# Optimization experiments

Hardware: AMD Instinct MI355X
Metric: run time of the kernel (lower is better)

The kernel has to match this reference:

```python
import jax, jax.numpy as jnp
import numpy as np

N_NODES = 50000
N_EDGES_UND = 400000
N_GRAPHS = 128
LATENT = 64
OUT_DIM = 64
NODE_F = 64
EDGE_F = 32
MAX_LV = 3


def setup_inputs() -> dict:
    key = jax.random.key(0)
    ks = jax.random.split(key, 12)
    rng = np.random.default_rng(0)
    # Build consistent directed edge list: each undirected pair (u,v) yields
    # directed edges e (u->v) and e+E_und (v->u); rev maps each to its twin.
    u = rng.integers(0, N_NODES, size=N_EDGES_UND)
    v = rng.integers(0, N_NODES, size=N_EDGES_UND)
    src = jnp.asarray(np.concatenate([u, v]), dtype=jnp.int32)
    dst = jnp.asarray(np.concatenate([v, u]), dtype=jnp.int32)
    e = np.arange(N_EDGES_UND)
    rev = jnp.asarray(np.concatenate([e + N_EDGES_UND, e]), dtype=jnp.int32)
    graph_ids = jnp.sort(jax.random.randint(ks[0], (N_NODES,), 0, N_GRAPHS)).astype(jnp.int32)
    s = 0.05
    return {
        'node_feat': jax.random.normal(ks[1], (N_NODES, NODE_F), jnp.float32),
        'edge_feat': jax.random.normal(ks[2], (2 * N_EDGES_UND, EDGE_F), jnp.float32),
        'src': src, 'dst': dst, 'rev': rev,
        'graph_ids': graph_ids, 'n_graphs': N_GRAPHS,
        'Wn': jax.random.normal(ks[3], (NODE_F, LATENT), jnp.float32) * s,
        'bn': jnp.zeros((LATENT,), jnp.float32),
        'We': jax.random.normal(ks[4], (EDGE_F, LATENT), jnp.float32) * s,
        'be': jnp.zeros((LATENT,), jnp.float32),
        'Wc': jax.random.normal(ks[5], (LATENT, LATENT), jnp.float32) * s,
        'bc': jnp.zeros((LATENT,), jnp.float32),
        'Wo': jax.random.normal(ks[6], (LATENT, OUT_DIM), jnp.float32) * s,
        'bo': jnp.zeros((OUT_DIM,), jnp.float32),
    }


def reference(node_feat, edge_feat, src, dst, rev, graph_ids, n_graphs,
              Wn, bn, We, be, Wc, bc, Wo, bo):
    n_nodes = node_feat.shape[0]
    # w_n2l / w_e2l
    input_node_linear = node_feat @ Wn + bn                  # [N, D]
    input_edge_linear = edge_feat @ We + be                  # [E, D]
    # n2e spmm: each directed edge gathers its source node's row
    input_message = input_edge_linear + input_node_linear[src]  # [E, D]
    cur = jax.nn.relu(input_message)
    # loopy BP: e2e spmm = (sum of messages into src node) - reverse-edge message
    for _ in range(MAX_LV):
        node_agg = jax.ops.segment_sum(cur, dst, num_segments=n_nodes)  # [N, D]
        e2epool = node_agg[src] - cur[rev]                              # [E, D]
        cur = jax.nn.relu(e2epool @ Wc + bc + input_message)
    # e2n spmm: sum incoming edge messages per node
    e2npool = jax.ops.segment_sum(cur, dst, num_segments=n_nodes)       # [N, D]
    hidden_msg = jax.nn.relu(e2npool)
    reluact = jax.nn.relu(hidden_msg @ Wo + bo)                         # [N, out]
    # subg spmm: sum node outputs per graph
    y = jax.ops.segment_sum(reluact, graph_ids, num_segments=n_graphs)  # [G, out]
    return jax.nn.relu(y)
```

## Files before the change

### kernel.cpp

```cpp
#include <hip/hip_runtime.h>


#define NN 50000
#define NE 800000
#define NG 128
#define D 64
#define LDE 36
#define LDW 66
#define LDO 72

typedef unsigned short u16;
typedef unsigned int u32;
typedef __bf16 bf16x8 __attribute__((ext_vector_type(8)));
typedef float f32x4 __attribute__((ext_vector_type(4)));

__device__ __forceinline__ float b2f(u16 u){ u32 x=((u32)u)<<16; float f; __builtin_memcpy(&f,&x,4); return f; }
__device__ __forceinline__ u16 f2b(float f){ u32 x; __builtin_memcpy(&x,&f,4); x += 0x7fffu + ((x>>16)&1u); return (u16)(x>>16); }
__device__ __forceinline__ u32 pack2(float a, float b){ return (u32)f2b(a) | ((u32)f2b(b)<<16); }
__device__ __forceinline__ void unpack8(uint4 v, float* o){
  o[0]=b2f((u16)(v.x&0xffffu)); o[1]=b2f((u16)(v.x>>16));
  o[2]=b2f((u16)(v.y&0xffffu)); o[3]=b2f((u16)(v.y>>16));
  o[4]=b2f((u16)(v.z&0xffffu)); o[5]=b2f((u16)(v.z>>16));
  o[6]=b2f((u16)(v.w&0xffffu)); o[7]=b2f((u16)(v.w>>16));
}

__global__ __launch_bounds__(256) void k_prep(const float* __restrict__ Wc, const float* __restrict__ We,
                                              u16* __restrict__ wcT, u16* __restrict__ weT){
  int i = blockIdx.x*256 + threadIdx.x;
  if (i < 4096){ int n=i>>6, k=i&63; wcT[i] = f2b(Wc[k*D+n]); }
  int j = i - 4096;
  if (j >= 0 && j < 2048){ int n=j>>5, k=j&31; weT[j] = f2b(We[k*D+n]); }
}

template<int ZERO>
__global__ __launch_bounds__(256) void k_cvt(const float* __restrict__ srcv, u16* __restrict__ dstb,
                                             float* __restrict__ zbuf){
  size_t i = (size_t)(blockIdx.x*256 + threadIdx.x)*4;
  float4 v = *(const float4*)(srcv + i);
  *(uint2*)(dstb + i) = make_uint2(pack2(v.x,v.y), pack2(v.z,v.w));
  if (ZERO) *(float4*)(zbuf + i) = make_float4(0.f,0.f,0.f,0.f);
}

__global__ __launch_bounds__(256) void k_inl(const float* __restrict__ nf, const float* __restrict__ Wn,
                                             const float* __restrict__ bn, u16* __restrict__ inlb){
  __shared__ float w[D*D];
  for (int i=threadIdx.x;i<D*D;i+=256) w[i]=Wn[i];
  __syncthreads();
  const int d = threadIdx.x&63;
  const int n = blockIdx.x*4 + (threadIdx.x>>6);
  if (n>=NN) return;
  float v = bn[d];
  const float* row = nf + (size_t)n*D;
  #pragma unroll 8
  for (int k=0;k<D;k++) v += row[k]*w[k*D+d];
  inlb[(size_t)n*D+d] = f2b(v);
}

__global__ __launch_bounds__(256) void k_im(const float* __restrict__ ef, const u16* __restrict__ weT,
                                            const float* __restrict__ be, const u16* __restrict__ inlb,
                                            const int* __restrict__ src, const int* __restrict__ perm,
                                            u16* __restrict__ imP){
  __shared__ __align__(16) u16 efs[64*LDE];
  __shared__ __align__(16) u16 wts[64*LDE];
  __shared__ float os[64*68];
  const int t = threadIdx.x;
  const int ebase = blockIdx.x*64;
  {
    int n=t&63, k0=(t>>6)*8;
    *(uint4*)&wts[n*LDE + k0] = *(const uint4*)(weT + n*32 + k0);
  }
  {
    int e=t>>2, k0=(t&3)*8;
    const float* p = ef + (size_t)(ebase+e)*32 + k0;
    float4 v0=*(const float4*)p, v1=*(const float4*)(p+4);
    uint4 pk = make_uint4(pack2(v0.x,v0.y),pack2(v0.z,v0.w),pack2(v1.x,v1.y),pack2(v1.z,v1.w));
    *(uint4*)&efs[e*LDE + k0] = pk;
  }
  __syncthreads();
  {
    int w=t>>6, lane=t&63, q=lane>>4, mr=lane&15;
    int rowb=w*16;
    bf16x8 A = *(const bf16x8*)&efs[(rowb+mr)*LDE + q*8];
    #pragma unroll
    for (int nt=0;nt<4;nt++){
      bf16x8 B = *(const bf16x8*)&wts[(nt*16+mr)*LDE + q*8];
      f32x4 acc = {0.f,0.f,0.f,0.f};
      acc = __builtin_amdgcn_mfma_f32_16x16x32_bf16(A,B,acc,0,0,0);
      #pragma unroll
      for (int r=0;r<4;r++) os[(rowb+q*4+r)*68 + nt*16+mr] = acc[r];
    }
  }
  {
    int e=t>>2, d0=(t&3)*16;
    const size_t eg = (size_t)(ebase+e);
    const int s = src[eg], ps = perm[eg];
    const u16* ip = inlb + (size_t)s*D + d0;
    uint4 iv0 = *(const uint4*)ip, iv1 = *(const uint4*)(ip+8);
    float il[16]; unpack8(iv0,il); unpack8(iv1,il+8);
    float x[16];
    #pragma unroll
    for (int j=0;j<16;j++) x[j] = os[e*68 + d0 + j] + be[d0+j] + il[j];
    uint4 p0 = make_uint4(pack2(x[0],x[1]),pack2(x[2],x[3]),pack2(x[4],x[5]),pack2(x[6],x[7]));
    uint4 p1 = make_uint4(pack2(x[8],x[9]),pack2(x[10],x[11]),pack2(x[12],x[13]),pack2(x[14],x[15]));
    u16* op = imP + (size_t)ps*D + d0;
    *(uint4*)op = p0; *(uint4*)(op+8) = p1;
  }
}

template<int MODE>
__global__ __launch_bounds__(256) void k_iter(const u16* __restrict__ imP, const u16* __restrict__ revIn,
      const u16* __restrict__ naWb, const u16* __restrict__ wcT, const float* __restrict__ bc,
      const int* __restrict__ srcP, const int* __restrict__ prevP, const int* __restrict__ nodeP,
      u16* __restrict__ revOut, float* __restrict__ naW_out){
  __shared__ __align__(16) u16 xs[64*LDW];
  __shared__ __align__(16) u16 wts[64*LDW];
  __shared__ __align__(16) u16 os[64*LDO];
  __shared__ int nid[64];
  const int t = threadIdx.x;
  const int lane = t&63, w = t>>6;
  const size_t sbase = (size_t)blockIdx.x*64;
  {
    const int k0 = w*16;
    *(uint4*)&wts[lane*LDW + k0]     = *(const uint4*)(wcT + lane*64 + k0);
    *(uint4*)&wts[lane*LDW + k0 + 8] = *(const uint4*)(wcT + lane*64 + k0 + 8);
  }
  if (lane < 16) nid[w*16 + lane] = nodeP[sbase + w*16 + lane];
  __syncthreads();
  {
    const int e = t>>2, d0 = (t&3)*16;
    const size_t slot = sbase + e;
    const u16* ip = imP + slot*D + d0;
    uint4 r0 = *(const uint4*)ip, r1 = *(const uint4*)(ip+8);
    float x[16]; unpack8(r0,x); unpack8(r1,x+8);
    if (MODE == 1){
      const int sp = srcP[slot];
      const u16* cp = revIn + slot*D + d0;
      uint4 c0=*(const uint4*)cp, c1=*(const uint4*)(cp+8);
      const u16* np_ = naWb + (size_t)sp*D + d0;
      uint4 n0=*(const uint4*)np_, n1=*(const uint4*)(np_+8);
      float cv[16], nv[16];
      unpack8(c0,cv); unpack8(c1,cv+8);
      unpack8(n0,nv); unpack8(n1,nv+8);
      #pragma unroll
      for (int j=0;j<16;j++) x[j] += nv[j] - cv[j] + bc[d0+j];
    }
    #pragma unroll
    for (int j=0;j<16;j++) x[j] = x[j]>0.f ? x[j] : 0.f;
    uint4 p0 = make_uint4(pack2(x[0],x[1]),pack2(x[2],x[3]),pack2(x[4],x[5]),pack2(x[6],x[7]));
    uint4 p1 = make_uint4(pack2(x[8],x[9]),pack2(x[10],x[11]),pack2(x[12],x[13]),pack2(x[14],x[15]));
    u16* qd = &xs[e*LDW + d0];
    *(uint4*)qd = p0; *(uint4*)(qd+8) = p1;
  }
  {
    const int q = lane>>4, mr = lane&15;
    const int rowb = w*16;
    bf16x8 A0 = *(const bf16x8*)&xs[(rowb+mr)*LDW + q*8];
    bf16x8 A1 = *(const bf16x8*)&xs[(rowb+mr)*LDW + 32 + q*8];
    #pragma unroll
    for (int nt=0;nt<4;nt++){
      bf16x8 B0 = *(const bf16x8*)&wts[(nt*16+mr)*LDW + q*8];
      bf16x8 B1 = *(const bf16x8*)&wts[(nt*16+mr)*LDW + 32 + q*8];
      f32x4 acc = {0.f,0.f,0.f,0.f};
      acc = __builtin_amdgcn_mfma_f32_16x16x32_bf16(A0,B0,acc,0,0,0);
      acc = __builtin_amdgcn_mfma_f32_16x16x32_bf16(A1,B1,acc,0,0,0);
      #pragma unroll
      for (int r=0;r<4;r++) os[(rowb+q*4+r)*LDO + nt*16 + mr] = f2b(acc[r]);
    }
    const int lr = lane>>2, cc = lane&3;
    const int tgt = prevP[sbase + rowb + lr];
    u16* gp = revOut + (size_t)tgt*D + cc*16;
    *(uint4*)gp     = *(const uint4*)&os[(rowb+lr)*LDO + cc*16];
    *(uint4*)(gp+8) = *(const uint4*)&os[(rowb+lr)*LDO + cc*16 + 8];
    float acc = 0.f;
    int curn = nid[rowb];
    #pragma unroll 4
    for (int i=0;i<16;++i){
      int n = nid[rowb+i];
      if (n != curn){
        atomicAdd(&naW_out[(size_t)curn*D + lane], acc);
        curn = n; acc = 0.f;
      }
      acc += b2f(os[(rowb+i)*LDO + lane]);
    }
    atomicAdd(&naW_out[(size_t)curn*D + lane], acc);
  }
}

__global__ __launch_bounds__(256) void k_last(const u16* __restrict__ imP, const u16* __restrict__ revIn,
      const u16* __restrict__ naWb, const float* __restrict__ bc,
      const int* __restrict__ srcP, const int* __restrict__ nodeP,
      float* __restrict__ e2n){
  __shared__ __align__(16) u16 xs[64*LDW];
  __shared__ int nid[64];
  const int t = threadIdx.x;
  const int lane = t&63, w = t>>6;
  const size_t sbase = (size_t)blockIdx.x*64;
  if (lane < 16) nid[w*16+lane] = nodeP[sbase + w*16 + lane];
  {
    const int e = t>>2, d0 = (t&3)*16;
    const size_t slot = sbase + e;
    const u16* ip = imP + slot*D + d0;
    uint4 r0 = *(const uint4*)ip, r1 = *(const uint4*)(ip+8);
    float x[16]; unpack8(r0,x); unpack8(r1,x+8);
    const int sp = srcP[slot];
    const u16* cp = revIn + slot*D + d0;
    uint4 c0 = *(const uint4*)cp, c1 = *(const uint4*)(cp+8);
    const u16* np_ = naWb + (size_t)sp*D + d0;
    uint4 n0 = *(const uint4*)np_, n1 = *(const uint4*)(np_+8);
    float cv[16], nv[16];
    unpack8(c0,cv); unpack8(c1,cv+8);
    unpack8(n0,nv); unpack8(n1,nv+8);
    #pragma unroll
    for (int j=0;j<16;j++){ x[j] += nv[j] - cv[j] + bc[d0+j]; x[j] = x[j]>0.f ? x[j] : 0.f; }
    uint4 p0 = make_uint4(pack2(x[0],x[1]),pack2(x[2],x[3]),pack2(x[4],x[5]),pack2(x[6],x[7]));
    uint4 p1 = make_uint4(pack2(x[8],x[9]),pack2(x[10],x[11]),pack2(x[12],x[13]),pack2(x[14],x[15]));
    u16* qd = &xs[e*LDW + d0];
    *(uint4*)qd = p0; *(uint4*)(qd+8) = p1;
  }
  {
    float acc = 0.f;
    int curn = nid[w*16];
    #pragma unroll 4
    for (int i=0;i<16;++i){
      int n = nid[w*16+i];
      if (n != curn){
        atomicAdd(&e2n[(size_t)curn*D + lane], acc);
        curn = n; acc = 0.f;
      }
      acc += b2f(xs[(w*16+i)*LDW + lane]);
    }
    atomicAdd(&e2n[(size_t)curn*D + lane], acc);
  }
}

__global__ void k_hist(const int* __restrict__ dst, int* __restrict__ cnt){
  int e = blockIdx.x*256 + threadIdx.x;
  atomicAdd(&cnt[dst[e]], 1);
}
__global__ __launch_bounds__(1024) void k_scan1(const int* __restrict__ cnt, int* __restrict__ outv,
                                                int* __restrict__ bsums, int n){
  __shared__ int sh[1024];
  int i = blockIdx.x*1024 + threadIdx.x;
  int v = (i<n)? cnt[i] : 0;
  sh[threadIdx.x]=v;
  __syncthreads();
  for (int off=1; off<1024; off<<=1){
    int tv = (threadIdx.x>=(unsigned)off)? sh[threadIdx.x-off] : 0;
    __syncthreads();
    sh[threadIdx.x] += tv;
    __syncthreads();
  }
  if (i<n) outv[i] = sh[threadIdx.x] - v;
  if (threadIdx.x==1023) bsums[blockIdx.x] = sh[1023];
}
__global__ __launch_bounds__(1024) void k_scan3(int* __restrict__ off, int* __restrict__ cur,
                                                const int* __restrict__ bsums, int n){
  __shared__ int spref;
  if (threadIdx.x < 64){
    int v = ((int)threadIdx.x < (int)blockIdx.x) ? bsums[threadIdx.x] : 0;
    #pragma unroll
    for (int o=1;o<64;o<<=1) v += __shfl_xor(v, o, 64);
    if (threadIdx.x==0) spref = v;
  }
  __syncthreads();
  int i = blockIdx.x*1024 + threadIdx.x;
  if (i<n){ int v = off[i] + spref; off[i]=v; cur[i]=v; }
}
__global__ void k_fill(const int* __restrict__ dst, const int* __restrict__ src,
                       int* __restrict__ cur, int* __restrict__ perm,
                       int* __restrict__ srcP, int* __restrict__ nodeP){
  int e = blockIdx.x*256 + threadIdx.x;
  int d = dst[e];
  int pos = atomicAdd(&cur[d], 1);
  perm[e] = pos;
  srcP[pos] = src[e];
  nodeP[pos] = d;
}
__global__ void k_prev(const int* __restrict__ rev, const int* __restrict__ perm, int* __restrict__ prevP){
  int e = blockIdx.x*256 + threadIdx.x;
  prevP[perm[e]] = perm[rev[e]];
}

__global__ __launch_bounds__(256) void k_final(const float* __restrict__ e2n, const float* __restrict__ Wo,
                                               const float* __restrict__ bo, const int* __restrict__ gid,
                                               float* __restrict__ yacc){
  __shared__ float w[D*D];
  for (int i=threadIdx.x;i<D*D;i+=256) w[i]=Wo[i];
  __syncthreads();
  const int d = threadIdx.x&63, sub = threadIdx.x>>6;
  const int n0 = blockIdx.x*32 + sub*8;
  const float bod = bo[d];
  float acc=0.f; int curg=-1;
  for (int i=0;i<8;i++){
    int n=n0+i;
    if (n>=NN) break;
    int g = gid[n];
    if (g!=curg){ if (curg>=0) atomicAdd(&yacc[curg*D+d], acc); curg=g; acc=0.f; }
    float v=bod;
    const float* er = e2n + (size_t)n*D;
    #pragma unroll 8
    for (int k=0;k<D;k++){ float h=er[k]; h = h>0.f?h:0.f; v += h*w[k*D+d]; }
    acc += (v>0.f ? v : 0.f);
  }
  if (curg>=0) atomicAdd(&yacc[curg*D+d], acc);
}
__global__ void k_out(const float* __restrict__ yacc, float* __restrict__ outp){
  int i = blockIdx.x*256 + threadIdx.x;
  if (i<NG*D){ float v=yacc[i]; outp[i]= v>0.f?v:0.f; }
}

static constexpr size_t SZ_E   = (size_t)NE*D*2;
static constexpr size_t SZ_NF4 = (size_t)NN*D*4;
static constexpr size_t SZ_NB  = (size_t)NN*D*2;
static constexpr size_t OFF_IMP  = 0;
static constexpr size_t OFF_RVA  = SZ_E;
static constexpr size_t OFF_RVB  = 2*SZ_E;
static constexpr size_t OFF_CCUR = 3*SZ_E;
static constexpr size_t OFF_NA0  = OFF_CCUR + 200064;
static constexpr size_t OFF_NA1  = OFF_NA0 + SZ_NF4;
static constexpr size_t OFF_E2N  = OFF_NA1 + SZ_NF4;
static constexpr size_t OFF_YACC = OFF_E2N + SZ_NF4;
static constexpr size_t ZERO_SZ  = 200064 + 3*SZ_NF4 + (size_t)NG*D*4;
static constexpr size_t OFF_NAB  = OFF_YACC + (size_t)NG*D*4;
static constexpr size_t OFF_INL  = OFF_NAB + SZ_NB;
static constexpr size_t OFF_COFF = OFF_INL + SZ_NB;
static constexpr size_t OFF_PERM = OFF_COFF + 200064;
static constexpr size_t OFF_SRCP = OFF_PERM + (size_t)NE*4;
static constexpr size_t OFF_PRVP = OFF_SRCP + (size_t)NE*4;
static constexpr size_t OFF_NODP = OFF_PRVP + (size_t)NE*4;
static constexpr size_t OFF_BS   = OFF_NODP + (size_t)NE*4;
static constexpr size_t OFF_WCT  = OFF_BS + 256;
static constexpr size_t OFF_WET  = OFF_WCT + 8192;

extern "C" void kernel_launch(void* const* d_in, const int* in_sizes, int n_in,
                              void* d_out, int out_size, void* d_ws, size_t ws_size,
                              hipStream_t stream) {
  const float* node_feat = (const float*)d_in[0];
  const float* edge_feat = (const float*)d_in[1];
  const int*   src       = (const int*)d_in[2];
  const int*   dst       = (const int*)d_in[3];
  const int*   rev       = (const int*)d_in[4];
  const int*   gid       = (const int*)d_in[5];
  const float* Wn = (const float*)d_in[7];
  const float* bn = (const float*)d_in[8];
  const float* We = (const float*)d_in[9];
  const float* be = (const float*)d_in[10];
  const float* Wc = (const float*)d_in[11];
  const float* bc = (const float*)d_in[12];
  const float* Wo = (const float*)d_in[13];
  const float* bo = (const float*)d_in[14];

  char* ws = (char*)d_ws;
  u16*   imP     = (u16*)(ws + OFF_IMP);
  u16*   revA    = (u16*)(ws + OFF_RVA);
  u16*   revB    = (u16*)(ws + OFF_RVB);
  float* naW0    = (float*)(ws + OFF_NA0);
  float* naW1    = (float*)(ws + OFF_NA1);
  float* e2n     = (float*)(ws + OFF_E2N);
  float* yacc    = (float*)(ws + OFF_YACC);
  u16*   naWb    = (u16*)(ws + OFF_NAB);
  u16*   inlb    = (u16*)(ws + OFF_INL);
  int*   csr_off = (int*)(ws + OFF_COFF);
  int*   csr_cur = (int*)(ws + OFF_CCUR);
  int*   perm    = (int*)(ws + OFF_PERM);
  int*   srcP    = (int*)(ws + OFF_SRCP);
  int*   prevP   = (int*)(ws + OFF_PRVP);
  int*   nodeP   = (int*)(ws + OFF_NODP);
  int*   bsums   = (int*)(ws + OFF_BS);
  u16*   wcT     = (u16*)(ws + OFF_WCT);
  u16*   weT     = (u16*)(ws + OFF_WET);

  hipMemsetAsync(ws + OFF_CCUR, 0, ZERO_SZ, stream);

  k_hist <<<NE/256, 256, 0, stream>>>(dst, csr_cur);
  k_scan1<<<49, 1024, 0, stream>>>(csr_cur, csr_off, bsums, NN);
  k_scan3<<<49, 1024, 0, stream>>>(csr_off, csr_cur, bsums, NN);
  k_fill <<<NE/256, 256, 0, stream>>>(dst, src, csr_cur, perm, srcP, nodeP);
  k_prev <<<NE/256, 256, 0, stream>>>(rev, perm, prevP);

  k_prep<<<24, 256, 0, stream>>>(Wc, We, wcT, weT);
  k_inl <<<NN/4, 256, 0, stream>>>(node_feat, Wn, bn, inlb);
  k_im  <<<NE/64, 256, 0, stream>>>(edge_feat, weT, be, inlb, src, perm, imP);

  k_iter<0><<<NE/64, 256, 0, stream>>>(imP, revA, naWb, wcT, bc, srcP, prevP, nodeP, revA, naW0);
  k_cvt<0><<<3125, 256, 0, stream>>>(naW0, naWb, (float*)nullptr);
  k_iter<1><<<NE/64, 256, 0, stream>>>(imP, revA, naWb, wcT, bc, srcP, prevP, nodeP, revB, naW1);
  k_cvt<1><<<3125, 256, 0, stream>>>(naW1, naWb, naW0);
  k_iter<1><<<NE/64, 256, 0, stream>>>(imP, revB, naWb, wcT, bc, srcP, prevP, nodeP, revA, naW0);
  k_cvt<0><<<3125, 256, 0, stream>>>(naW0, naWb, (float*)nullptr);
  k_last<<<NE/64, 256, 0, stream>>>(imP, revA, naWb, bc, srcP, nodeP, e2n);

  k_final<<<(NN+31)/32, 256, 0, stream>>>(e2n, Wo, bo, gid, yacc);
  k_out<<<(NG*D)/256, 256, 0, stream>>>(yacc, (float*)d_out);
}
```

Baseline: 681.2 us.

## Drop bf16 node-aggregate conversion kernels and read MFMA weight fragments from global

Removes the three k_cvt passes that turned the fp32 node aggregates into bf16. The iteration kernels now gather the fp32 aggregate rows directly, and a memset zeroes the reused buffer instead. The weight matrices are prepacked in MFMA fragment order so each lane loads its B operand straight from global/L2, which drops the per-block shared-memory staging and a __syncthreads. The trade is twice the bytes per random node gather (fp32 instead of bf16) in exchange for fewer launches and full passes over the aggregate buffer.

Result: slower. 706.0 us (+3.6%).

```diff
diff --git a/kernel.cpp b/kernel.cpp
--- a/kernel.cpp
+++ b/kernel.cpp
@@ -25,20 +25,24 @@
 }
 
 __global__ __launch_bounds__(256) void k_prep(const float* __restrict__ Wc, const float* __restrict__ We,
-                                              u16* __restrict__ wcT, u16* __restrict__ weT){
+                                              u16* __restrict__ wcB, u16* __restrict__ weB){
   int i = blockIdx.x*256 + threadIdx.x;
-  if (i < 4096){ int n=i>>6, k=i&63; wcT[i] = f2b(Wc[k*D+n]); }
-  int j = i - 4096;
-  if (j >= 0 && j < 2048){ int n=j>>5, k=j&31; weT[j] = f2b(We[k*D+n]); }
-}
-
-template<int ZERO>
-__global__ __launch_bounds__(256) void k_cvt(const float* __restrict__ srcv, u16* __restrict__ dstb,
-                                             float* __restrict__ zbuf){
-  size_t i = (size_t)(blockIdx.x*256 + threadIdx.x)*4;
-  float4 v = *(const float4*)(srcv + i);
-  *(uint2*)(dstb + i) = make_uint2(pack2(v.x,v.y), pack2(v.z,v.w));
-  if (ZERO) *(float4*)(zbuf + i) = make_float4(0.f,0.f,0.f,0.f);
+  if (i < 4096){
+    int nt = i>>10, r = i&1023;
+    int h = r>>9, r2 = r&511;
+    int j = r2>>3, kk = r2&7;
+    int row = nt*16 + (j&15);
+    int k = h*32 + (j>>4)*8 + kk;
+    wcB[i] = f2b(Wc[k*D + row]);
+  }
+  int t = i - 4096;
+  if (t >= 0 && t < 2048){
+    int nt = t>>9, r = t&511;
+    int j = r>>3, kk = r&7;
+    int row = nt*16 + (j&15);
+    int k = (j>>4)*8 + kk;
+    weB[t] = f2b(We[k*D + row]);
+  }
 }
 
 __global__ __launch_bounds__(256) void k_inl(const float* __restrict__ nf, const float* __restrict__ Wn,
@@ -56,19 +60,14 @@
   inlb[(size_t)n*D+d] = f2b(v);
 }
 
-__global__ __launch_bounds__(256) void k_im(const float* __restrict__ ef, const u16* __restrict__ weT,
+__global__ __launch_bounds__(256) void k_im(const float* __restrict__ ef, const u16* __restrict__ weB,
                                             const float* __restrict__ be, const u16* __restrict__ inlb,
                                             const int* __restrict__ src, const int* __restrict__ perm,
                                             u16* __restrict__ imP){
   __shared__ __align__(16) u16 efs[64*LDE];
-  __shared__ __align__(16) u16 wts[64*LDE];
   __shared__ float os[64*68];
   const int t = threadIdx.x;
   const int ebase = blockIdx.x*64;
-  {
-    int n=t&63, k0=(t>>6)*8;
-    *(uint4*)&wts[n*LDE + k0] = *(const uint4*)(weT + n*32 + k0);
-  }
   {
     int e=t>>2, k0=(t&3)*8;
     const float* p = ef + (size_t)(ebase+e)*32 + k0;
@@ -76,14 +75,13 @@
     uint4 pk = make_uint4(pack2(v0.x,v0.y),pack2(v0.z,v0.w),pack2(v1.x,v1.y),pack2(v1.z,v1.w));
     *(uint4*)&efs[e*LDE + k0] = pk;
   }
-  __syncthreads();
   {
     int w=t>>6, lane=t&63, q=lane>>4, mr=lane&15;
     int rowb=w*16;
     bf16x8 A = *(const bf16x8*)&efs[(rowb+mr)*LDE + q*8];
     #pragma unroll
     for (int nt=0;nt<4;nt++){
-      bf16x8 B = *(const bf16x8*)&wts[(nt*16+mr)*LDE + q*8];
+      bf16x8 B = *(const bf16x8*)(weB + nt*512 + lane*8);
       f32x4 acc = {0.f,0.f,0.f,0.f};
       acc = __builtin_amdgcn_mfma_f32_16x16x32_bf16(A,B,acc,0,0,0);
       #pragma unroll
@@ -109,23 +107,16 @@
 
 template<int MODE>
 __global__ __launch_bounds__(256) void k_iter(const u16* __restrict__ imP, const u16* __restrict__ revIn,
-      const u16* __restrict__ naWb, const u16* __restrict__ wcT, const float* __restrict__ bc,
+      const float* __restrict__ naW, const u16* __restrict__ wcB, const float* __restrict__ bc,
       const int* __restrict__ srcP, const int* __restrict__ prevP, const int* __restrict__ nodeP,
       u16* __restrict__ revOut, float* __restrict__ naW_out){
   __shared__ __align__(16) u16 xs[64*LDW];
-  __shared__ __align__(16) u16 wts[64*LDW];
   __shared__ __align__(16) u16 os[64*LDO];
   __shared__ int nid[64];
   const int t = threadIdx.x;
   const int lane = t&63, w = t>>6;
   const size_t sbase = (size_t)blockIdx.x*64;
-  {
-    const int k0 = w*16;
-    *(uint4*)&wts[lane*LDW + k0]     = *(const uint4*)(wcT + lane*64 + k0);
-    *(uint4*)&wts[lane*LDW + k0 + 8] = *(const uint4*)(wcT + lane*64 + k0 + 8);
-  }
   if (lane < 16) nid[w*16 + lane] = nodeP[sbase + w*16 + lane];
-  __syncthreads();
   {
     const int e = t>>2, d0 = (t&3)*16;
     const size_t slot = sbase + e;
@@ -136,11 +127,15 @@
       const int sp = srcP[slot];
       const u16* cp = revIn + slot*D + d0;
       uint4 c0=*(const uint4*)cp, c1=*(const uint4*)(cp+8);
-      const u16* np_ = naWb + (size_t)sp*D + d0;
-      uint4 n0=*(const uint4*)np_, n1=*(const uint4*)(np_+8);
-      float cv[16], nv[16];
+      float nv[16];
+      { const float* np_ = naW + (size_t)sp*D + d0;
+        *(float4*)&nv[0]  = *(const float4*)np_;
+        *(float4*)&nv[4]  = *(const float4*)(np_+4);
+        *(float4*)&nv[8]  = *(const float4*)(np_+8);
+        *(float4*)&nv[12] = *(const float4*)(np_+12);
+      }
+      float cv[16];
       unpack8(c0,cv); unpack8(c1,cv+8);
-      unpack8(n0,nv); unpack8(n1,nv+8);
       #pragma unroll
       for (int j=0;j<16;j++) x[j] += nv[j] - cv[j] + bc[d0+j];
     }
@@ -158,8 +153,8 @@
     bf16x8 A1 = *(const bf16x8*)&xs[(rowb+mr)*LDW + 32 + q*8];
     #pragma unroll
     for (int nt=0;nt<4;nt++){
-      bf16x8 B0 = *(const bf16x8*)&wts[(nt*16+mr)*LDW + q*8];
-      bf16x8 B1 = *(const bf16x8*)&wts[(nt*16+mr)*LDW + 32 + q*8];
+      bf16x8 B0 = *(const bf16x8*)(wcB + nt*1024 + lane*8);
+      bf16x8 B1 = *(const bf16x8*)(wcB + nt*1024 + 512 + lane*8);
       f32x4 acc = {0.f,0.f,0.f,0.f};
       acc = __builtin_amdgcn_mfma_f32_16x16x32_bf16(A0,B0,acc,0,0,0);
       acc = __builtin_amdgcn_mfma_f32_16x16x32_bf16(A1,B1,acc,0,0,0);
@@ -187,7 +182,7 @@
 }
 
 __global__ __launch_bounds__(256) void k_last(const u16* __restrict__ imP, const u16* __restrict__ revIn,
-      const u16* __restrict__ naWb, const float* __restrict__ bc,
+      const float* __restrict__ naW, const float* __restrict__ bc,
       const int* __restrict__ srcP, const int* __restrict__ nodeP,
       float* __restrict__ e2n){
   __shared__ __align__(16) u16 xs[64*LDW];
@@ -205,11 +200,15 @@
     const int sp = srcP[slot];
     const u16* cp = revIn + slot*D + d0;
     uint4 c0 = *(const uint4*)cp, c1 = *(const uint4*)(cp+8);
-    const u16* np_ = naWb + (size_t)sp*D + d0;
-    uint4 n0 = *(const uint4*)np_, n1 = *(const uint4*)(np_+8);
-    float cv[16], nv[16];
+    float nv[16];
+    { const float* np_ = naW + (size_t)sp*D + d0;
+      *(float4*)&nv[0]  = *(const float4*)np_;
+      *(float4*)&nv[4]  = *(const float4*)(np_+4);
+      *(float4*)&nv[8]  = *(const float4*)(np_+8);
+      *(float4*)&nv[12] = *(const float4*)(np_+12);
+    }
+    float cv[16];
     unpack8(c0,cv); unpack8(c1,cv+8);
-    unpack8(n0,nv); unpack8(n1,nv+8);
     #pragma unroll
     for (int j=0;j<16;j++){ x[j] += nv[j] - cv[j] + bc[d0+j]; x[j] = x[j]>0.f ? x[j] : 0.f; }
     uint4 p0 = make_uint4(pack2(x[0],x[1]),pack2(x[2],x[3]),pack2(x[4],x[5]),pack2(x[6],x[7]));
@@ -358,7 +357,6 @@
   float* naW1    = (float*)(ws + OFF_NA1);
   float* e2n     = (float*)(ws + OFF_E2N);
   float* yacc    = (float*)(ws + OFF_YACC);
-  u16*   naWb    = (u16*)(ws + OFF_NAB);
   u16*   inlb    = (u16*)(ws + OFF_INL);
   int*   csr_off = (int*)(ws + OFF_COFF);
   int*   csr_cur = (int*)(ws + OFF_CCUR);
@@ -367,8 +365,8 @@
   int*   prevP   = (int*)(ws + OFF_PRVP);
   int*   nodeP   = (int*)(ws + OFF_NODP);
   int*   bsums   = (int*)(ws + OFF_BS);
-  u16*   wcT     = (u16*)(ws + OFF_WCT);
-  u16*   weT     = (u16*)(ws + OFF_WET);
+  u16*   wcB     = (u16*)(ws + OFF_WCT);
+  u16*   weB     = (u16*)(ws + OFF_WET);
 
   hipMemsetAsync(ws + OFF_CCUR, 0, ZERO_SZ, stream);
 
@@ -378,17 +376,15 @@
   k_fill <<<NE/256, 256, 0, stream>>>(dst, src, csr_cur, perm, srcP, nodeP);
   k_prev <<<NE/256, 256, 0, stream>>>(rev, perm, prevP);
 
-  k_prep<<<24, 256, 0, stream>>>(Wc, We, wcT, weT);
+  k_prep<<<24, 256, 0, stream>>>(Wc, We, wcB, weB);
   k_inl <<<NN/4, 256, 0, stream>>>(node_feat, Wn, bn, inlb);
-  k_im  <<<NE/64, 256, 0, stream>>>(edge_feat, weT, be, inlb, src, perm, imP);
-
-  k_iter<0><<<NE/64, 256, 0, stream>>>(imP, revA, naWb, wcT, bc, srcP, prevP, nodeP, revA, naW0);
-  k_cvt<0><<<3125, 256, 0, stream>>>(naW0, naWb, (float*)nullptr);
-  k_iter<1><<<NE/64, 256, 0, stream>>>(imP, revA, naWb, wcT, bc, srcP, prevP, nodeP, revB, naW1);
-  k_cvt<1><<<3125, 256, 0, stream>>>(naW1, naWb, naW0);
-  k_iter<1><<<NE/64, 256, 0, stream>>>(imP, revB, naWb, wcT, bc, srcP, prevP, nodeP, revA, naW0);
-  k_cvt<0><<<3125, 256, 0, stream>>>(naW0, naWb, (float*)nullptr);
-  k_last<<<NE/64, 256, 0, stream>>>(imP, revA, naWb, bc, srcP, nodeP, e2n);
+  k_im  <<<NE/64, 256, 0, stream>>>(edge_feat, weB, be, inlb, src, perm, imP);
+
+  k_iter<0><<<NE/64, 256, 0, stream>>>(imP, revA, naW1, wcB, bc, srcP, prevP, nodeP, revA, naW0);
+  k_iter<1><<<NE/64, 256, 0, stream>>>(imP, revA, naW0, wcB, bc, srcP, prevP, nodeP, revB, naW1);
+  hipMemsetAsync(ws + OFF_NA0, 0, SZ_NF4, stream);
+  k_iter<1><<<NE/64, 256, 0, stream>>>(imP, revB, naW1, wcB, bc, srcP, prevP, nodeP, revA, naW0);
+  k_last<<<NE/64, 256, 0, stream>>>(imP, revA, naW0, bc, srcP, nodeP, e2n);
 
   k_final<<<(NN+31)/32, 256, 0, stream>>>(e2n, Wo, bo, gid, yacc);
   k_out<<<(NG*D)/256, 256, 0, stream>>>(yacc, (float*)d_out);
```
